# Optimization experiments

Hardware: AMD Instinct MI355X
Metric: run time of the kernel (lower is better)

The kernel has to match this reference:

```python
import jax, jax.numpy as jnp
import numpy as np

DIM = 1536; NH = 12; HD = DIM // NH; C = HD // 2  # C = 64
F, H, W = 12, 16, 16; S = F * H * W  # 3072 tokens
NFPB = 3       # num_frame_per_block (block-causal granularity)
LOCAL = 6      # local_attn_size in frames
SINK = 1       # sink_size in frames
EPS = 1e-06


def setup_inputs():
    key = jax.random.key(0)
    ks = jax.random.split(key, 6)
    sc = 1.0 / np.sqrt(DIM)
    x = jax.random.normal(ks[0], (1, S, DIM), jnp.float32)
    Wq = jax.random.normal(ks[1], (DIM, DIM), jnp.float32) * sc
    Wk = jax.random.normal(ks[2], (DIM, DIM), jnp.float32) * sc
    Wv = jax.random.normal(ks[3], (DIM, DIM), jnp.float32) * sc
    Wo = jax.random.normal(ks[4], (DIM, DIM), jnp.float32) * sc
    zeros = jnp.zeros((DIM,), jnp.float32); ones = jnp.ones((DIM,), jnp.float32)
    # RoPE table: unit-modulus complex freqs stored as cos/sin, shape [1024, C]
    ang = jax.random.uniform(ks[5], (1024, C), jnp.float32) * (2.0 * np.pi)
    return dict(x=x, Wq=Wq, bq=zeros, Wk=Wk, bk=zeros, Wv=Wv, bv=zeros,
                Wo=Wo, bo=zeros, gq=ones, gk=ones,
                freqs_cos=jnp.cos(ang), freqs_sin=jnp.sin(ang), f=F, h=H, w=W)


def _rms_norm(x, g):
    y = x * jax.lax.rsqrt(jnp.mean(x * x, axis=-1, keepdims=True) + EPS)
    return y * g


def _pos_table(tab, f, h, w):
    # split [1024, C] into frame/height/width parts and broadcast to [f*h*w, C]
    cf = C - 2 * (C // 3); ch = C // 3
    tf = jnp.broadcast_to(tab[:f, :cf][:, None, None, :], (f, h, w, cf))
    th = jnp.broadcast_to(tab[:h, cf:cf + ch][None, :, None, :], (f, h, w, ch))
    tw = jnp.broadcast_to(tab[:w, cf + ch:][None, None, :, :], (f, h, w, ch))
    return jnp.concatenate([tf, th, tw], axis=-1).reshape(f * h * w, C)


def _rope(x, cosp, sinp):
    # complex multiply on consecutive (real, imag) pairs along head_dim
    b, s, n, d = x.shape
    xp = x.reshape(b, s, n, d // 2, 2)
    xr, xi = xp[..., 0], xp[..., 1]
    cp = cosp[None, :, None, :]; sp = sinp[None, :, None, :]
    out = jnp.stack([xr * cp - xi * sp, xr * sp + xi * cp], axis=-1)
    return out.reshape(b, s, n, d)


def reference(x, Wq, bq, Wk, bk, Wv, bv, Wo, bo, gq, gk, freqs_cos, freqs_sin, f, h, w):
    b, s, _ = x.shape
    q = _rms_norm(x @ Wq.T + bq, gq).reshape(b, s, NH, HD)
    k = _rms_norm(x @ Wk.T + bk, gk).reshape(b, s, NH, HD)
    v = (x @ Wv.T + bv).reshape(b, s, NH, HD)
    cosp = _pos_table(freqs_cos, f, h, w)
    sinp = _pos_table(freqs_sin, f, h, w)
    rq = _rope(q, cosp, sinp)
    rk = _rope(k, cosp, sinp)
    # block mask: block-causal (bidirectional inside a frame-block) + local window + sink
    idx = jnp.arange(s)
    frame = idx // (h * w)
    blk = frame // NFPB
    qb, kb = blk[:, None], blk[None, :]
    mask = (kb <= qb) & ((((qb - kb) * NFPB) < LOCAL) | (frame[None, :] < SINK))
    scores = jnp.einsum('bqnd,bknd->bnqk', rq, rk) * (HD ** -0.5)
    scores = jnp.where(mask[None, None], scores, jnp.finfo(scores.dtype).min)
    probs = jax.nn.softmax(scores, axis=-1)
    out = jnp.einsum('bnqk,bknd->bqnd', probs, v).reshape(b, s, DIM)
    return out @ Wo.T + bo
```

## Files before the change

### kernel.cpp

```cpp
#include <hip/hip_runtime.h>
#include <stdint.h>

typedef unsigned short u16;
typedef __attribute__((ext_vector_type(8))) short bf16x8;
typedef __attribute__((ext_vector_type(4))) short bf16x4;
typedef __attribute__((ext_vector_type(4))) float f32x4;

constexpr int DMODEL = 1536;
constexpr int SEQ    = 3072;
constexpr int NHEAD  = 12;
constexpr int HDIM   = 128;

__device__ __forceinline__ u16 f2bf(float f){
  union { float f; unsigned u; } v; v.f = f;
  return (u16)((v.u + 0x7fffu + ((v.u >> 16) & 1u)) >> 16);
}

__global__ __launch_bounds__(256) void cvt_all(
    const float* __restrict__ x,  const float* __restrict__ wq,
    const float* __restrict__ wk, const float* __restrict__ wv, const float* __restrict__ wo,
    u16* __restrict__ xb, u16* __restrict__ wqb, u16* __restrict__ wkb,
    u16* __restrict__ wvb, u16* __restrict__ wob)
{
  const int NX = (SEQ * DMODEL) / 4;
  const int NW = (DMODEL * DMODEL) / 4;
  int i = blockIdx.x * 256 + threadIdx.x;
  const float* src; u16* dst; int off;
  if      (i < NX)          { src = x;  dst = xb;  off = i; }
  else if (i < NX + NW)     { src = wq; dst = wqb; off = i - NX; }
  else if (i < NX + 2 * NW) { src = wk; dst = wkb; off = i - NX - NW; }
  else if (i < NX + 3 * NW) { src = wv; dst = wvb; off = i - NX - 2 * NW; }
  else                      { src = wo; dst = wob; off = i - NX - 3 * NW; }
  float4 f = ((const float4*)src)[off];
  ushort4 o;
  o.x = f2bf(f.x); o.y = f2bf(f.y); o.z = f2bf(f.z); o.w = f2bf(f.w);
  ((ushort4*)dst)[off] = o;
}

__device__ __forceinline__ void gload16(const u16* g, u16* l){
  __builtin_amdgcn_global_load_lds((const __attribute__((address_space(1))) void*)g,
                                   (__attribute__((address_space(3))) void*)l, 16, 0, 0);
}

__device__ __forceinline__ void gemm_core(const u16* __restrict__ A, const u16* __restrict__ W,
    const float* __restrict__ bias, float* __restrict__ C, u16* __restrict__ VT,
    int m0, int n0, bool vfuse, u16* As, u16* Bs)
{
  const int tid  = threadIdx.x;
  const int lane = tid & 63;
  const int wv   = tid >> 6;
  const int wm   = wv & 1, wn = wv >> 1;
  const int l15  = lane & 15, lg = lane >> 4;

  f32x4 acc[4][4];
#pragma unroll
  for (int i = 0; i < 4; i++)
#pragma unroll
    for (int j = 0; j < 4; j++){ f32x4 z = {0.f,0.f,0.f,0.f}; acc[i][j] = z; }

  const int r0 = wv * 16 + (lane >> 2);
  const int r1 = (wv + 4) * 16 + (lane >> 2);
  const int cc = (lane & 3) * 8;
  const u16* Ab = A + (size_t)m0 * DMODEL;
  const u16* Wb = W + (size_t)n0 * DMODEL;

  auto stageg = [&](int b, int k0){
    gload16(Ab + (size_t)r0 * DMODEL + k0 + cc, As + b * 4096 + wv * 512);
    gload16(Ab + (size_t)r1 * DMODEL + k0 + cc, As + b * 4096 + (wv + 4) * 512);
    gload16(Wb + (size_t)r0 * DMODEL + k0 + cc, Bs + b * 4096 + wv * 512);
    gload16(Wb + (size_t)r1 * DMODEL + k0 + cc, Bs + b * 4096 + (wv + 4) * 512);
  };

  stageg(0, 0);
  __syncthreads();

  for (int k0 = 0; k0 < DMODEL; k0 += 32){
    int b = (k0 >> 5) & 1;
    if (k0 + 32 < DMODEL) stageg(b ^ 1, k0 + 32);

    const u16* Ar = As + b * 4096;
    const u16* Br = Bs + b * 4096;
    bf16x8 af[4], bfr[4];
#pragma unroll
    for (int mi = 0; mi < 4; mi++)
      af[mi]  = *(const bf16x8*)(Ar + (wm * 64 + mi * 16 + l15) * 32 + lg * 8);
#pragma unroll
    for (int ni = 0; ni < 4; ni++)
      bfr[ni] = *(const bf16x8*)(Br + (wn * 64 + ni * 16 + l15) * 32 + lg * 8);
#pragma unroll
    for (int mi = 0; mi < 4; mi++)
#pragma unroll
      for (int ni = 0; ni < 4; ni++)
        acc[mi][ni] = __builtin_amdgcn_mfma_f32_16x16x32_bf16(af[mi], bfr[ni], acc[mi][ni], 0, 0, 0);
    __syncthreads();
  }

  if (!vfuse){
#pragma unroll
    for (int mi = 0; mi < 4; mi++){
      int row = m0 + wm * 64 + mi * 16 + (lg << 2);
#pragma unroll
      for (int ni = 0; ni < 4; ni++){
        int col = n0 + wn * 64 + ni * 16 + l15;
        float bvv = bias[col];
#pragma unroll
        for (int r = 0; r < 4; r++)
          C[(size_t)(row + r) * DMODEL + col] = acc[mi][ni][r] + bvv;
      }
    }
  } else {
#pragma unroll
    for (int mi = 0; mi < 4; mi++){
      int gbase = m0 + wm * 64 + (mi >> 1) * 32 + lg * 8 + (mi & 1) * 4;
#pragma unroll
      for (int ni = 0; ni < 4; ni++){
        int d = n0 + wn * 64 + ni * 16 + l15;
        float bvv = bias[d];
        ushort4 o;
        o.x = f2bf(acc[mi][ni][0] + bvv);
        o.y = f2bf(acc[mi][ni][1] + bvv);
        o.z = f2bf(acc[mi][ni][2] + bvv);
        o.w = f2bf(acc[mi][ni][3] + bvv);
        *(ushort4*)(VT + (size_t)d * SEQ + gbase) = o;
      }
    }
  }
}

__global__ __launch_bounds__(256) void gemm_qkv(const u16* __restrict__ xb,
    const u16* __restrict__ wqb, const u16* __restrict__ wkb, const u16* __restrict__ wvb,
    const float* __restrict__ bq, const float* __restrict__ bk, const float* __restrict__ bv,
    float* __restrict__ qf, float* __restrict__ kf, u16* __restrict__ vt)
{
  __shared__ u16 As[2 * 4096], Bs[2 * 4096];
  int mt = blockIdx.x, nt = blockIdx.y;
  int sel = nt / 12, ntl = nt % 12;
  const u16* W = sel == 0 ? wqb : (sel == 1 ? wkb : wvb);
  const float* bias = sel == 0 ? bq : (sel == 1 ? bk : bv);
  float* C = sel == 0 ? qf : kf;
  gemm_core(xb, W, bias, C, vt, mt * 128, ntl * 128, sel == 2, As, Bs);
}

__global__ __launch_bounds__(256) void gemm_o(const u16* __restrict__ ab,
    const u16* __restrict__ wob, const float* __restrict__ bo, float* __restrict__ out)
{
  __shared__ u16 As[2 * 4096], Bs[2 * 4096];
  gemm_core(ab, wob, bo, out, nullptr, blockIdx.x * 128, blockIdx.y * 128, false, As, Bs);
}

__global__ __launch_bounds__(256) void rmsrope_kernel(
    const float* __restrict__ qin, const float* __restrict__ kin,
    const float* __restrict__ gq, const float* __restrict__ gk,
    const float* __restrict__ fcos, const float* __restrict__ fsin,
    u16* __restrict__ rq, u16* __restrict__ rk)
{
  int gw   = (blockIdx.x * 256 + threadIdx.x) >> 6;
  int lane = threadIdx.x & 63;
  int s    = gw >> 1;
  int pass = gw & 1;
  const float* in = pass ? kin : qin;
  const float* g  = pass ? gk  : gq;
  u16* outp       = pass ? rk  : rq;

  const float* row = in + (size_t)s * DMODEL + lane * 24;
  float v[24];
#pragma unroll
  for (int j = 0; j < 6; j++) *(float4*)(v + 4 * j) = ((const float4*)row)[j];

  float ss = 0.f;
#pragma unroll
  for (int j = 0; j < 24; j++) ss += v[j] * v[j];
#pragma unroll
  for (int m = 1; m < 64; m <<= 1) ss += __shfl_xor(ss, m);
  float scale = rsqrtf(ss * (1.0f / (float)DMODEL) + 1e-6f);

  float gv[24];
  const float* gp = g + lane * 24;
#pragma unroll
  for (int j = 0; j < 6; j++) *(float4*)(gv + 4 * j) = ((const float4*)gp)[j];

  int fi = s >> 8, hi2 = (s >> 4) & 15, wi = s & 15;
  u16 o[24];
#pragma unroll
  for (int jp = 0; jp < 12; jp++){
    int i  = lane * 12 + jp;
    int pi = i & 63;
    int idx = pi < 22 ? fi : (pi < 43 ? hi2 : wi);
    float cv = fcos[idx * 64 + pi];
    float sv = fsin[idx * 64 + pi];
    float xr = v[2 * jp]     * scale * gv[2 * jp];
    float xi = v[2 * jp + 1] * scale * gv[2 * jp + 1];
    o[2 * jp]     = f2bf(xr * cv - xi * sv);
    o[2 * jp + 1] = f2bf(xr * sv + xi * cv);
  }
  u16* op = outp + (size_t)s * DMODEL + lane * 24;
#pragma unroll
  for (int j = 0; j < 3; j++) *(bf16x8*)(op + 8 * j) = *(bf16x8*)(o + 8 * j);
}

__global__ __launch_bounds__(256, 2) void attn_kernel(const u16* __restrict__ rq,
    const u16* __restrict__ rk, const u16* __restrict__ vt,
    float* __restrict__ pO, float* __restrict__ pl)
{
  __shared__ u16 Ks[2][8192];
  __shared__ u16 Vs[2][8192];

  const int tid  = threadIdx.x;
  const int lane = tid & 63;
  const int wv   = tid >> 6;
  const int head = blockIdx.y;
  const int bid  = blockIdx.x;
  int qb, blk, sub;
  if      (bid < 24){ qb = 3; blk = bid >> 1;        sub = bid & 1; }
  else if (bid < 48){ qb = 2; blk = (bid - 24) >> 1; sub = bid & 1; }
  else if (bid < 72){ qb = 1; blk = (bid - 48) >> 1; sub = bid & 1; }
  else              { qb = 0; blk = bid - 72;        sub = 0; }
  const int qblk = qb * 12 + blk;
  const int q0   = qblk * 64 + wv * 16;
  const int l15  = lane & 15, lg = lane >> 4;
  const int swz  = (l15 & 7) << 4;
  const float sc = 0.08838834764831845f;

  int r1s = 0, r1e = 0, r0e = 0;
  if      (qb == 0){ r0e = 768; }
  else if (qb == 1){ r0e = 1536; }
  else if (qb == 2){ r0e = 256; r1s = 768;  r1e = 2304; }
  else             { r0e = 256; r1s = 1536; r1e = 3072; }
  const int nt0 = r0e >> 6;
  const int nt  = nt0 + ((r1e - r1s) >> 6);
  const int hl  = (qb == 0) ? nt : (nt >> 1);
  const int ts  = sub * hl, te = ts + hl;

  const char* rkB = (const char*)rk;
  const char* vtB = (const char*)vt;
  auto k0_of = [&](int t){ return t < nt0 ? t * 64 : (r1s + (t - nt0) * 64); };

  auto stage = [&](int buf, int k0){
    char* Kd = (char*)Ks[buf];
    char* Vd = (char*)Vs[buf];
#pragma unroll
    for (int c = 0; c < 4; c++){
      int o = c * 4096 + wv * 1024 + lane * 16;
      int row = o >> 8, colb = o & 255;
      gload16((const u16*)(rkB + (size_t)(k0 + row) * (DMODEL * 2) + head * (HDIM * 2)
                               + (colb ^ ((row & 7) << 4))),
              (u16*)(Kd + c * 4096 + wv * 1024));
    }
#pragma unroll
    for (int c = 0; c < 4; c++){
      int o = c * 4096 + wv * 1024 + lane * 16;
      int row = o >> 7, colb = o & 127;
      gload16((const u16*)(vtB + (size_t)(head * HDIM + row) * (SEQ * 2) + (size_t)k0 * 2
                               + (colb ^ ((row & 7) << 4))),
              (u16*)(Vd + c * 4096 + wv * 1024));
    }
  };

  bf16x8 qfr[4];
  const u16* qbase = rq + (size_t)(q0 + l15) * DMODEL + head * HDIM + lg * 8;
#pragma unroll
  for (int c = 0; c < 4; c++) qfr[c] = *(const bf16x8*)(qbase + c * 32);

  f32x4 oacc[8];
#pragma unroll
  for (int i = 0; i < 8; i++){ f32x4 z = {0.f,0.f,0.f,0.f}; oacc[i] = z; }
  float l_run = 0.f;

  stage(0, k0_of(ts));
  __syncthreads();

  for (int t = ts; t < te; t++){
    int buf = (t - ts) & 1;
    if (t + 1 < te) stage(buf ^ 1, k0_of(t + 1));

    const char* Kb = (const char*)Ks[buf];
    const char* Vb = (const char*)Vs[buf];
#pragma unroll
    for (int half = 0; half < 2; half++){
      const int kt = half * 32;
      const char* kr0 = Kb + (kt + l15) * 256;
      const char* kr1 = kr0 + 16 * 256;
      bf16x8 kf0[4], kf1[4];
#pragma unroll
      for (int c = 0; c < 4; c++){
        kf0[c] = *(const bf16x8*)(kr0 + ((lg * 16 + c * 64) ^ swz));
        kf1[c] = *(const bf16x8*)(kr1 + ((lg * 16 + c * 64) ^ swz));
      }
      f32x4 s0 = {0.f,0.f,0.f,0.f}, s1 = {0.f,0.f,0.f,0.f};
      __builtin_amdgcn_s_setprio(1);
#pragma unroll
      for (int c = 0; c < 4; c++){
        s0 = __builtin_amdgcn_mfma_f32_16x16x32_bf16(kf0[c], qfr[c], s0, 0, 0, 0);
        s1 = __builtin_amdgcn_mfma_f32_16x16x32_bf16(kf1[c], qfr[c], s1, 0, 0, 0);
      }
      __builtin_amdgcn_s_setprio(0);

      bf16x8 pf;
      float lsum = 0.f;
#pragma unroll
      for (int r = 0; r < 4; r++){
        float e0 = __expf(fmaf(s0[r], sc, -12.f));
        float e1 = __expf(fmaf(s1[r], sc, -12.f));
        lsum += e0 + e1;
        pf[r]     = (short)f2bf(e0);
        pf[r + 4] = (short)f2bf(e1);
      }
      l_run += lsum;

      __builtin_amdgcn_s_setprio(1);
#pragma unroll
      for (int ch = 0; ch < 8; ch++){
        bf16x8 vf8 = *(const bf16x8*)(Vb + (ch * 16 + l15) * 128 + ((half * 64 + lg * 16) ^ swz));
        oacc[ch] = __builtin_amdgcn_mfma_f32_16x16x32_bf16(pf, vf8, oacc[ch], 0, 0, 0);
      }
      __builtin_amdgcn_s_setprio(0);
    }
    __syncthreads();
  }

  const size_t punit = (size_t)(head * 84 + bid);
  l_run += __shfl_xor(l_run, 16);
  l_run += __shfl_xor(l_run, 32);
  if (lg == 0) pl[punit * 64 + wv * 16 + l15] = l_run;

  float* po = pO + punit * 8192;
#pragma unroll
  for (int ch = 0; ch < 8; ch++)
#pragma unroll
    for (int r = 0; r < 4; r++)
      po[(wv * 16 + lg * 4 + r) * 128 + ch * 16 + l15] = oacc[ch][r];
}

__global__ __launch_bounds__(256) void attn_reduce(const float* __restrict__ pO,
    const float* __restrict__ pl, u16* __restrict__ ao)
{
  const int qblk = blockIdx.x;
  const int head = blockIdx.y;
  const int qb = qblk / 12, blk = qblk % 12;
  int b0, nu;
  if      (qb == 0){ b0 = 72 + blk;     nu = 1; }
  else if (qb == 1){ b0 = 48 + 2 * blk; nu = 2; }
  else if (qb == 2){ b0 = 24 + 2 * blk; nu = 2; }
  else             { b0 = 2 * blk;      nu = 2; }
  const size_t u0 = (size_t)(head * 84 + b0);
  const float* O0 = pO + u0 * 8192;
  const float* L0 = pl + u0 * 64;

  __shared__ float ls[64];
  int t = threadIdx.x;
  if (t < 64) ls[t] = L0[t] + (nu == 2 ? L0[64 + t] : 0.f);
  __syncthreads();

  int q = t >> 2, dc = (t & 3) * 32;
  float inv = 1.f / ls[q];
  const float* a0 = O0 + q * 128 + dc;
  const float* a1 = a0 + 8192;
  u16 buf[32];
#pragma unroll
  for (int j = 0; j < 32; j += 4){
    float4 xv = *(const float4*)(a0 + j);
    if (nu == 2){
      float4 y = *(const float4*)(a1 + j);
      xv.x += y.x; xv.y += y.y; xv.z += y.z; xv.w += y.w;
    }
    buf[j]     = f2bf(xv.x * inv);
    buf[j + 1] = f2bf(xv.y * inv);
    buf[j + 2] = f2bf(xv.z * inv);
    buf[j + 3] = f2bf(xv.w * inv);
  }
  u16* op = ao + (size_t)(qblk * 64 + q) * DMODEL + head * HDIM + dc;
#pragma unroll
  for (int j = 0; j < 32; j += 8) *(bf16x8*)(op + j) = *(bf16x8*)(buf + j);
}

extern "C" void kernel_launch(void* const* d_in, const int* in_sizes, int n_in,
                              void* d_out, int out_size, void* d_ws, size_t ws_size,
                              hipStream_t stream)
{
  const float* x    = (const float*)d_in[0];
  const float* Wq   = (const float*)d_in[1];
  const float* bq   = (const float*)d_in[2];
  const float* Wk   = (const float*)d_in[3];
  const float* bk   = (const float*)d_in[4];
  const float* Wv   = (const float*)d_in[5];
  const float* bv   = (const float*)d_in[6];
  const float* Wo   = (const float*)d_in[7];
  const float* bo   = (const float*)d_in[8];
  const float* gq   = (const float*)d_in[9];
  const float* gk   = (const float*)d_in[10];
  const float* fcos = (const float*)d_in[11];
  const float* fsin = (const float*)d_in[12];
  float* out = (float*)d_out;

  char* ws = (char*)d_ws;
  size_t off = 0;
  auto alloc = [&](size_t bytes){
    void* p = ws + off;
    off += (bytes + 255) & ~(size_t)255;
    return p;
  };
  const size_t SD = (size_t)SEQ * DMODEL;
  const size_t WW = (size_t)DMODEL * DMODEL;
  u16*   xb  = (u16*)  alloc(SD * 2);
  u16*   wqb = (u16*)  alloc(WW * 2);
  u16*   wkb = (u16*)  alloc(WW * 2);
  u16*   wvb = (u16*)  alloc(WW * 2);
  u16*   wob = (u16*)  alloc(WW * 2);
  float* qf  = (float*)alloc(SD * 4);
  float* kf  = (float*)alloc(SD * 4);
  u16*   rq  = (u16*)  alloc(SD * 2);
  u16*   rk  = (u16*)  alloc(SD * 2);
  u16*   vt  = (u16*)  alloc(SD * 2);
  u16*   ao  = (u16*)  alloc(SD * 2);
  float* pl  = (float*)alloc((size_t)1008 * 64 * 4);
  float* pO  = qf;

  const int NX = (SEQ * DMODEL) / 4, NW = (DMODEL * DMODEL) / 4;
  cvt_all<<<(NX + 4 * NW) / 256, 256, 0, stream>>>(x, Wq, Wk, Wv, Wo, xb, wqb, wkb, wvb, wob);
  gemm_qkv<<<dim3(SEQ / 128, 36), 256, 0, stream>>>(xb, wqb, wkb, wvb, bq, bk, bv, qf, kf, vt);
  rmsrope_kernel<<<(SEQ * 2) / 4, 256, 0, stream>>>(qf, kf, gq, gk, fcos, fsin, rq, rk);
  attn_kernel<<<dim3(84, NHEAD), 256, 0, stream>>>(rq, rk, vt, pO, pl);
  attn_reduce<<<dim3(48, NHEAD), 256, 0, stream>>>(pO, pl, ao);
  gemm_o<<<dim3(SEQ / 128, DMODEL / 128), 256, 0, stream>>>(ao, wob, bo, out);
}
```

Before: 321.7 us.

## Replace QKV GEMM with 256x256-tile, swizzled-LDS, 8-wave pipelined kernel

Replaces the 128x128-tile QKV projection GEMM with a dedicated kernel using 256x256 output tiles, 512 threads, K-step 64, an XOR-swizzled LDS layout, and staggered prefetch of A and B between MFMA quarter-phases with setprio and explicit barriers. It also remaps block IDs into XCD-aware groups over a flat 216-block grid. The goal is higher arithmetic intensity per tile, fewer LDS bank conflicts and better overlap of global loads with MFMA work in the largest GEMM. In exchange it uses more LDS (128KB) and more registers, which may limit occupancy, and 216 blocks on 256 CUs leaves some CUs idle.

```diff
diff --git a/kernel.cpp b/kernel.cpp
--- a/kernel.cpp
+++ b/kernel.cpp
@@ -42,63 +42,130 @@
                                    (__attribute__((address_space(3))) void*)l, 16, 0, 0);
 }
 
-__device__ __forceinline__ void gemm_core(const u16* __restrict__ A, const u16* __restrict__ W,
-    const float* __restrict__ bias, float* __restrict__ C, u16* __restrict__ VT,
-    int m0, int n0, bool vfuse, u16* As, u16* Bs)
-{
+__global__ __launch_bounds__(512, 2) void gemm_qkv256(const u16* __restrict__ xb,
+    const u16* __restrict__ wqb, const u16* __restrict__ wkb, const u16* __restrict__ wvb,
+    const float* __restrict__ bq, const float* __restrict__ bk, const float* __restrict__ bv,
+    float* __restrict__ qf, float* __restrict__ kf, u16* __restrict__ vt)
+{
+  __shared__ u16 lds[2][2][16384];
+
   const int tid  = threadIdx.x;
   const int lane = tid & 63;
-  const int wv   = tid >> 6;
-  const int wm   = wv & 1, wn = wv >> 1;
+  const int wid  = tid >> 6;
+  const int wm   = wid >> 2;
+  const int wn   = wid & 3;
   const int l15  = lane & 15, lg = lane >> 4;
-
-  f32x4 acc[4][4];
-#pragma unroll
-  for (int i = 0; i < 4; i++)
+  const int swz  = (l15 & 7) << 4;
+
+  const int bid  = blockIdx.x;
+  const int sbid = (bid & 7) * 27 + (bid >> 3);
+  const int mt   = sbid / 18, nt = sbid % 18;
+  const int sel  = nt / 6, ntl = nt % 6;
+  const u16* W = sel == 0 ? wqb : (sel == 1 ? wkb : wvb);
+  const float* bias = sel == 0 ? bq : (sel == 1 ? bk : bv);
+  const int m0 = mt * 256, n0 = ntl * 256;
+
+  const char* Ag = (const char*)(xb + (size_t)m0 * DMODEL);
+  const char* Bg = (const char*)(W  + (size_t)n0 * DMODEL);
+
+  auto stage_op = [&](int buf, int op, const char* G, int kt){
+#pragma unroll
+    for (int c = 0; c < 4; c++){
+      int ob  = c * 8192 + wid * 1024 + lane * 16;
+      int row = ob >> 7, colb = ob & 127;
+      gload16((const u16*)(G + (size_t)row * (DMODEL * 2) + (size_t)kt * 128
+                             + (colb ^ ((row & 7) << 4))),
+              (u16*)((char*)&lds[buf][op][0] + c * 8192 + wid * 1024));
+    }
+  };
+
+  f32x4 acc[8][4];
+#pragma unroll
+  for (int i = 0; i < 8; i++)
 #pragma unroll
     for (int j = 0; j < 4; j++){ f32x4 z = {0.f,0.f,0.f,0.f}; acc[i][j] = z; }
 
-  const int r0 = wv * 16 + (lane >> 2);
-  const int r1 = (wv + 4) * 16 + (lane >> 2);
-  const int cc = (lane & 3) * 8;
-  const u16* Ab = A + (size_t)m0 * DMODEL;
-  const u16* Wb = W + (size_t)n0 * DMODEL;
-
-  auto stageg = [&](int b, int k0){
-    gload16(Ab + (size_t)r0 * DMODEL + k0 + cc, As + b * 4096 + wv * 512);
-    gload16(Ab + (size_t)r1 * DMODEL + k0 + cc, As + b * 4096 + (wv + 4) * 512);
-    gload16(Wb + (size_t)r0 * DMODEL + k0 + cc, Bs + b * 4096 + wv * 512);
-    gload16(Wb + (size_t)r1 * DMODEL + k0 + cc, Bs + b * 4096 + (wv + 4) * 512);
-  };
-
-  stageg(0, 0);
-  __syncthreads();
-
-  for (int k0 = 0; k0 < DMODEL; k0 += 32){
-    int b = (k0 >> 5) & 1;
-    if (k0 + 32 < DMODEL) stageg(b ^ 1, k0 + 32);
-
-    const u16* Ar = As + b * 4096;
-    const u16* Br = Bs + b * 4096;
-    bf16x8 af[4], bfr[4];
-#pragma unroll
-    for (int mi = 0; mi < 4; mi++)
-      af[mi]  = *(const bf16x8*)(Ar + (wm * 64 + mi * 16 + l15) * 32 + lg * 8);
-#pragma unroll
-    for (int ni = 0; ni < 4; ni++)
-      bfr[ni] = *(const bf16x8*)(Br + (wn * 64 + ni * 16 + l15) * 32 + lg * 8);
-#pragma unroll
-    for (int mi = 0; mi < 4; mi++)
+  const int NK = DMODEL / 64;
+
+  stage_op(0, 0, Ag, 0);
+  stage_op(0, 1, Bg, 0);
+  asm volatile("s_waitcnt vmcnt(0)" ::: "memory");
+  __builtin_amdgcn_sched_barrier(0);
+  __builtin_amdgcn_s_barrier();
+  __builtin_amdgcn_sched_barrier(0);
+
+#pragma unroll 1
+  for (int t = 0; t < NK; t++){
+    const int b = t & 1;
+    const char* Abase = (const char*)&lds[b][0][0];
+    const char* Bbase = (const char*)&lds[b][1][0];
+    bf16x8 bfr[4][2], afr[2][2];
+
+#pragma unroll
+    for (int ni = 0; ni < 4; ni++){
+      int rb = wn * 64 + ni * 16 + l15;
+#pragma unroll
+      for (int ks = 0; ks < 2; ks++)
+        bfr[ni][ks] = *(const bf16x8*)(Bbase + rb * 128 + ((ks * 64 + lg * 16) ^ swz));
+    }
+#pragma unroll
+    for (int i = 0; i < 2; i++){
+      int ra = wm * 128 + i * 16 + l15;
+#pragma unroll
+      for (int ks = 0; ks < 2; ks++)
+        afr[i][ks] = *(const bf16x8*)(Abase + ra * 128 + ((ks * 64 + lg * 16) ^ swz));
+    }
+    if (t + 1 < NK) stage_op(b ^ 1, 0, Ag, t + 1);
+    __builtin_amdgcn_sched_barrier(0);
+    __builtin_amdgcn_s_barrier();
+    __builtin_amdgcn_sched_barrier(0);
+    __builtin_amdgcn_s_setprio(1);
+#pragma unroll
+    for (int i = 0; i < 2; i++)
 #pragma unroll
       for (int ni = 0; ni < 4; ni++)
-        acc[mi][ni] = __builtin_amdgcn_mfma_f32_16x16x32_bf16(af[mi], bfr[ni], acc[mi][ni], 0, 0, 0);
-    __syncthreads();
-  }
-
-  if (!vfuse){
-#pragma unroll
-    for (int mi = 0; mi < 4; mi++){
-      int row = m0 + wm * 64 + mi * 16 + (lg << 2);
+#pragma unroll
+        for (int ks = 0; ks < 2; ks++)
+          acc[i][ni] = __builtin_amdgcn_mfma_f32_16x16x32_bf16(afr[i][ks], bfr[ni][ks], acc[i][ni], 0, 0, 0);
+    __builtin_amdgcn_s_setprio(0);
+    __builtin_amdgcn_sched_barrier(0);
+    __builtin_amdgcn_s_barrier();
+    __builtin_amdgcn_sched_barrier(0);
+
+#pragma unroll
+    for (int qd = 1; qd < 4; qd++){
+#pragma unroll
+      for (int i = 0; i < 2; i++){
+        int ra = wm * 128 + (qd * 2 + i) * 16 + l15;
+#pragma unroll
+        for (int ks = 0; ks < 2; ks++)
+          afr[i][ks] = *(const bf16x8*)(Abase + ra * 128 + ((ks * 64 + lg * 16) ^ swz));
+      }
+      if (qd == 1 && t + 1 < NK) stage_op(b ^ 1, 1, Bg, t + 1);
+      __builtin_amdgcn_sched_barrier(0);
+      __builtin_amdgcn_s_barrier();
+      __builtin_amdgcn_sched_barrier(0);
+      __builtin_amdgcn_s_setprio(1);
+#pragma unroll
+      for (int i = 0; i < 2; i++)
+#pragma unroll
+        for (int ni = 0; ni < 4; ni++)
+#pragma unroll
+          for (int ks = 0; ks < 2; ks++)
+            acc[qd * 2 + i][ni] = __builtin_amdgcn_mfma_f32_16x16x32_bf16(afr[i][ks], bfr[ni][ks], acc[qd * 2 + i][ni], 0, 0, 0);
+      __builtin_amdgcn_s_setprio(0);
+      if (qd == 3) asm volatile("s_waitcnt vmcnt(0)" ::: "memory");
+      __builtin_amdgcn_sched_barrier(0);
+      __builtin_amdgcn_s_barrier();
+      __builtin_amdgcn_sched_barrier(0);
+    }
+  }
+
+  if (sel != 2){
+    float* C = sel == 0 ? qf : kf;
+#pragma unroll
+    for (int mi = 0; mi < 8; mi++){
+      int row = m0 + wm * 128 + mi * 16 + lg * 4;
 #pragma unroll
       for (int ni = 0; ni < 4; ni++){
         int col = n0 + wn * 64 + ni * 16 + l15;
@@ -110,8 +177,8 @@
     }
   } else {
 #pragma unroll
-    for (int mi = 0; mi < 4; mi++){
-      int gbase = m0 + wm * 64 + (mi >> 1) * 32 + lg * 8 + (mi & 1) * 4;
+    for (int mi = 0; mi < 8; mi++){
+      int gbase = m0 + wm * 128 + (mi >> 1) * 32 + lg * 8 + (mi & 1) * 4;
 #pragma unroll
       for (int ni = 0; ni < 4; ni++){
         int d = n0 + wn * 64 + ni * 16 + l15;
@@ -121,31 +188,84 @@
         o.y = f2bf(acc[mi][ni][1] + bvv);
         o.z = f2bf(acc[mi][ni][2] + bvv);
         o.w = f2bf(acc[mi][ni][3] + bvv);
-        *(ushort4*)(VT + (size_t)d * SEQ + gbase) = o;
-      }
-    }
-  }
-}
-
-__global__ __launch_bounds__(256) void gemm_qkv(const u16* __restrict__ xb,
-    const u16* __restrict__ wqb, const u16* __restrict__ wkb, const u16* __restrict__ wvb,
-    const float* __restrict__ bq, const float* __restrict__ bk, const float* __restrict__ bv,
-    float* __restrict__ qf, float* __restrict__ kf, u16* __restrict__ vt)
-{
-  __shared__ u16 As[2 * 4096], Bs[2 * 4096];
-  int mt = blockIdx.x, nt = blockIdx.y;
-  int sel = nt / 12, ntl = nt % 12;
-  const u16* W = sel == 0 ? wqb : (sel == 1 ? wkb : wvb);
-  const float* bias = sel == 0 ? bq : (sel == 1 ? bk : bv);
-  float* C = sel == 0 ? qf : kf;
-  gemm_core(xb, W, bias, C, vt, mt * 128, ntl * 128, sel == 2, As, Bs);
+        *(ushort4*)(vt + (size_t)d * SEQ + gbase) = o;
+      }
+    }
+  }
+}
+
+__device__ __forceinline__ void gemm_core(const u16* __restrict__ A, const u16* __restrict__ W,
+    const float* __restrict__ bias, float* __restrict__ C, int m0, int n0,
+    u16* As, u16* Bs)
+{
+  const int tid  = threadIdx.x;
+  const int lane = tid & 63;
+  const int wv   = tid >> 6;
+  const int wm   = wv & 1, wn = wv >> 1;
+  const int l15  = lane & 15, lg = lane >> 4;
+
+  f32x4 acc[4][4];
+#pragma unroll
+  for (int i = 0; i < 4; i++)
+#pragma unroll
+    for (int j = 0; j < 4; j++){ f32x4 z = {0.f,0.f,0.f,0.f}; acc[i][j] = z; }
+
+  const int r0 = wv * 16 + (lane >> 2);
+  const int r1 = (wv + 4) * 16 + (lane >> 2);
+  const int cc = (lane & 3) * 8;
+  const u16* Ab = A + (size_t)m0 * DMODEL;
+  const u16* Wb = W + (size_t)n0 * DMODEL;
+
+  auto stageg = [&](int b, int k0){
+    gload16(Ab + (size_t)r0 * DMODEL + k0 + cc, As + b * 4096 + wv * 512);
+    gload16(Ab + (size_t)r1 * DMODEL + k0 + cc, As + b * 4096 + (wv + 4) * 512);
+    gload16(Wb + (size_t)r0 * DMODEL + k0 + cc, Bs + b * 4096 + wv * 512);
+    gload16(Wb + (size_t)r1 * DMODEL + k0 + cc, Bs + b * 4096 + (wv + 4) * 512);
+  };
+
+  stageg(0, 0);
+  __syncthreads();
+
+  for (int k0 = 0; k0 < DMODEL; k0 += 32){
+    int b = (k0 >> 5) & 1;
+    if (k0 + 32 < DMODEL) stageg(b ^ 1, k0 + 32);
+
+    const u16* Ar = As + b * 4096;
+    const u16* Br = Bs + b * 4096;
+    bf16x8 af[4], bfr[4];
+#pragma unroll
+    for (int mi = 0; mi < 4; mi++)
+      af[mi]  = *(const bf16x8*)(Ar + (wm * 64 + mi * 16 + l15) * 32 + lg * 8);
+#pragma unroll
+    for (int ni = 0; ni < 4; ni++)
+      bfr[ni] = *(const bf16x8*)(Br + (wn * 64 + ni * 16 + l15) * 32 + lg * 8);
+#pragma unroll
+    for (int mi = 0; mi < 4; mi++)
+#pragma unroll
+      for (int ni = 0; ni < 4; ni++)
+        acc[mi][ni] = __builtin_amdgcn_mfma_f32_16x16x32_bf16(af[mi], bfr[ni], acc[mi][ni], 0, 0, 0);
+    __syncthreads();
+  }
+
+#pragma unroll
+  for (int mi = 0; mi < 4; mi++){
+    int row = m0 + wm * 64 + mi * 16 + (lg << 2);
+#pragma unroll
+    for (int ni = 0; ni < 4; ni++){
+      int col = n0 + wn * 64 + ni * 16 + l15;
+      float bvv = bias[col];
+#pragma unroll
+      for (int r = 0; r < 4; r++)
+        C[(size_t)(row + r) * DMODEL + col] = acc[mi][ni][r] + bvv;
+    }
+  }
 }
 
 __global__ __launch_bounds__(256) void gemm_o(const u16* __restrict__ ab,
     const u16* __restrict__ wob, const float* __restrict__ bo, float* __restrict__ out)
 {
   __shared__ u16 As[2 * 4096], Bs[2 * 4096];
-  gemm_core(ab, wob, bo, out, nullptr, blockIdx.x * 128, blockIdx.y * 128, false, As, Bs);
+  gemm_core(ab, wob, bo, out, blockIdx.x * 128, blockIdx.y * 128, As, Bs);
 }
 
 __global__ __launch_bounds__(256) void rmsrope_kernel(
@@ -417,7 +537,7 @@
 
   const int NX = (SEQ * DMODEL) / 4, NW = (DMODEL * DMODEL) / 4;
   cvt_all<<<(NX + 4 * NW) / 256, 256, 0, stream>>>(x, Wq, Wk, Wv, Wo, xb, wqb, wkb, wvb, wob);
-  gemm_qkv<<<dim3(SEQ / 128, 36), 256, 0, stream>>>(xb, wqb, wkb, wvb, bq, bk, bv, qf, kf, vt);
+  gemm_qkv256<<<216, 512, 0, stream>>>(xb, wqb, wkb, wvb, bq, bk, bv, qf, kf, vt);
   rmsrope_kernel<<<(SEQ * 2) / 4, 256, 0, stream>>>(qf, kf, gq, gk, fcos, fsin, rq, rk);
   attn_kernel<<<dim3(84, NHEAD), 256, 0, stream>>>(rq, rk, vt, pO, pl);
   attn_reduce<<<dim3(48, NHEAD), 256, 0, stream>>>(pO, pl, ao);
```

Result: faster. 289.9 us (-9.9%).
